# Kernel optimization log

Hardware: AMD Instinct MI355X
Metric: run time of the kernel (lower is better)

Reference implementation:

```python
import jax, jax.numpy as jnp
import numpy as np

WML, B, S, D = 64, 64, 40, 512  # word_max_len, batch, sents_max_len, dim


def setup_inputs() -> dict:
    key = jax.random.key(0)
    ks = jax.random.split(key, 8)
    source = jax.random.normal(ks[0], (B, D), dtype=jnp.float32)
    word_bank = jax.random.normal(ks[1], (WML, B, S, D), dtype=jnp.float32)
    # per-sentence word counts in [1, WML] so every sentence has >=1 valid token
    word_lengths = jax.random.randint(ks[2], (B, S), 1, WML + 1)
    sent_bank = jax.random.normal(ks[3], (S, B, D), dtype=jnp.float32)
    sent_lengths = jax.random.randint(ks[4], (B,), 1, S + 1)  # unused by forward math
    static_attn = jax.random.uniform(ks[5], (B, S), dtype=jnp.float32)
    scale = 1.0 / np.sqrt(D)
    W_word = jax.random.normal(ks[6], (D, D), dtype=jnp.float32) * scale
    W_sent = jax.random.normal(ks[7], (D, D), dtype=jnp.float32) * scale
    W_out = jax.random.normal(jax.random.fold_in(key, 99), (D, 2 * D), dtype=jnp.float32) * scale
    return {"source": source, "word_bank": word_bank, "word_lengths": word_lengths,
            "sent_bank": sent_bank, "sent_lengths": sent_lengths, "static_attn": static_attn,
            "W_word": W_word, "W_sent": W_sent, "W_out": W_out}


def reference(source, word_bank, word_lengths, sent_bank, sent_lengths, static_attn, W_word, W_sent, W_out):
    wml, batch, sents, dim = word_bank.shape
    # [wml, B, S, D] -> [B, S, wml, D] -> [B, S*wml, D]  (matches torch transpose chain)
    wb = jnp.transpose(word_bank, (1, 2, 0, 3)).reshape(batch, sents * wml, dim)
    # score(source, wb, 'word'): (source @ W_word^T) dotted with each word vector
    word_align = jnp.einsum('bd,bnd->bn', source @ W_word.T, wb)          # [B, S*wml]
    sb = jnp.transpose(sent_bank, (1, 0, 2))                               # [B, S, D]
    sent_align = jnp.einsum('bd,bsd->bs', source @ W_sent.T, sb)          # [B, S]
    # triple product: word score * sentence score * static attention
    align = (word_align.reshape(batch, sents, wml)
             * (sent_align * static_attn)[:, :, None]).reshape(batch, sents * wml)
    # sequence mask per sentence, flattened to [B, S*wml]
    mask = (jnp.arange(wml)[None, None, :] < word_lengths[:, :, None]).reshape(batch, sents * wml)
    align = jnp.where(mask, align, -jnp.inf)
    align_vectors = jax.nn.softmax(align, axis=-1) + 1e-20               # [B, S*wml]
    c = jnp.einsum('bn,bnd->bd', align_vectors, wb)                       # [B, D]
    attn_h = jnp.tanh(jnp.concatenate([c, source], axis=-1) @ W_out.T)    # [B, D]
    return attn_h, align_vectors
```

## Files before the change

kernel.cpp:

```cpp
#include <hip/hip_runtime.h>
#include <math.h>

#define BB   64
#define SS   40
#define WMLC 64
#define DD   512
#define NN   2560
#define NBLK 20
#define WPB  4
#define NWAVES (NBLK*WPB)
#define RPW (NN/NWAVES)
#define L2E 1.4426950408889634f

__device__ __forceinline__ float wave_reduce_sum(float v) {
    #pragma unroll
    for (int off = 32; off > 0; off >>= 1) v += __shfl_xor(v, off, 64);
    return v;
}

__global__ __launch_bounds__(256) void k_proj(const float* __restrict__ src,
                                              const float* __restrict__ Ww,
                                              const float* __restrict__ Ws,
                                              float* __restrict__ qw,
                                              float* __restrict__ qs) {
    __shared__ float xs[DD];
    const int b = blockIdx.y;
    const int t = threadIdx.x;
    const float* W = blockIdx.x ? Ws : Ww;
    float* q = blockIdx.x ? qs : qw;
    ((float2*)xs)[t] = ((const float2*)(src + b * DD))[t];
    __syncthreads();
    const float* r0 = W + (size_t)t * DD;
    const float* r1 = W + (size_t)(t + 256) * DD;
    float acc0 = 0.f, acc1 = 0.f;
    for (int k = 0; k < DD; k += 4) {
        float4 x  = *(const float4*)(xs + k);
        float4 w0 = *(const float4*)(r0 + k);
        float4 w1 = *(const float4*)(r1 + k);
        acc0 += x.x * w0.x + x.y * w0.y + x.z * w0.z + x.w * w0.w;
        acc1 += x.x * w1.x + x.y * w1.y + x.z * w1.z + x.w * w1.w;
    }
    q[b * DD + t] = acc0;
    q[b * DD + t + 256] = acc1;
}

__global__ __launch_bounds__(256) void k_sstat(const float* __restrict__ qs,
                                               const float* __restrict__ sb,
                                               const float* __restrict__ sa,
                                               float* __restrict__ sstat) {
    const int b = blockIdx.x;
    const int t = threadIdx.x, wave = t >> 6, lane = t & 63;
    const int d0 = lane * 4, d1 = 256 + lane * 4;
    const float4 q0 = *(const float4*)(qs + b * DD + d0);
    const float4 q1 = *(const float4*)(qs + b * DD + d1);
    for (int j = 0; j < SS / WPB; ++j) {
        const int s = wave * (SS / WPB) + j;
        const float* row = sb + ((size_t)s * BB + b) * DD;
        float4 a0 = *(const float4*)(row + d0);
        float4 a1 = *(const float4*)(row + d1);
        float p = a0.x * q0.x + a0.y * q0.y + a0.z * q0.z + a0.w * q0.w
                + a1.x * q1.x + a1.y * q1.y + a1.z * q1.z + a1.w * q1.w;
        p = wave_reduce_sum(p);
        if (lane == 0) sstat[b * SS + s] = p * sa[b * SS + s];
    }
}

__global__ __launch_bounds__(256) void k_main(const float* __restrict__ wb,
                                              const float* __restrict__ qw,
                                              const float* __restrict__ sstat,
                                              const int* __restrict__ wl,
                                              float* __restrict__ scores,
                                              float* __restrict__ part_c,
                                              float* __restrict__ part_ml) {
    const int b = blockIdx.y;
    const int chunk = blockIdx.x;
    const int t = threadIdx.x, wave = t >> 6, lane = t & 63;
    const int gw = chunk * WPB + wave;
    const int d0 = lane * 4, d1 = 256 + lane * 4;
    const float4 q0 = *(const float4*)(qw + b * DD + d0);
    const float4 q1 = *(const float4*)(qw + b * DD + d1);

    float m = -INFINITY, l = 0.f;
    float4 c0 = {0.f, 0.f, 0.f, 0.f}, c1 = {0.f, 0.f, 0.f, 0.f};

    for (int k = 0; k < RPW; ++k) {
        const int n = gw + k * NWAVES;
        const int s = n >> 6, w = n & 63;
        if (w >= wl[b * SS + s]) continue;
        const float* row = wb + (size_t)(((w * BB + b) * SS + s)) * DD;
        float4 a0 = *(const float4*)(row + d0);
        float4 a1 = *(const float4*)(row + d1);
        float p = a0.x * q0.x + a0.y * q0.y + a0.z * q0.z + a0.w * q0.w
                + a1.x * q1.x + a1.y * q1.y + a1.z * q1.z + a1.w * q1.w;
        p = wave_reduce_sum(p);
        const float a = p * sstat[b * SS + s];
        if (lane == 0) scores[b * NN + n] = a;
        if (a > m) {
            const float sc = (m == -INFINITY) ? 0.f : exp2f((m - a) * L2E);
            l *= sc;
            c0.x *= sc; c0.y *= sc; c0.z *= sc; c0.w *= sc;
            c1.x *= sc; c1.y *= sc; c1.z *= sc; c1.w *= sc;
            m = a;
        }
        const float e = exp2f((a - m) * L2E);
        l += e;
        c0.x += e * a0.x; c0.y += e * a0.y; c0.z += e * a0.z; c0.w += e * a0.w;
        c1.x += e * a1.x; c1.y += e * a1.y; c1.z += e * a1.z; c1.w += e * a1.w;
    }

    __shared__ float s_m[WPB], s_l[WPB];
    __shared__ float s_c[WPB][DD];
    *(float4*)(&s_c[wave][d0]) = c0;
    *(float4*)(&s_c[wave][d1]) = c1;
    if (lane == 0) { s_m[wave] = m; s_l[wave] = l; }
    __syncthreads();
    const float mb = fmaxf(fmaxf(s_m[0], s_m[1]), fmaxf(s_m[2], s_m[3]));
    float lb = 0.f, cA = 0.f, cB = 0.f;
    #pragma unroll
    for (int wv = 0; wv < WPB; ++wv) {
        const float mi = s_m[wv];
        const float sc = (mi == -INFINITY) ? 0.f : exp2f((mi - mb) * L2E);
        lb += s_l[wv] * sc;
        cA += s_c[wv][t] * sc;
        cB += s_c[wv][t + 256] * sc;
    }
    const int pidx = b * NBLK + chunk;
    part_c[(size_t)pidx * DD + t] = cA;
    part_c[(size_t)pidx * DD + t + 256] = cB;
    if (t == 0) { part_ml[pidx * 2] = mb; part_ml[pidx * 2 + 1] = lb; }
}

__global__ __launch_bounds__(256) void k_reduce(const float* __restrict__ part_c,
                                                const float* __restrict__ part_ml,
                                                float* __restrict__ c_final,
                                                float* __restrict__ mz) {
    const int b = blockIdx.x, t = threadIdx.x;
    float mg = -INFINITY;
    for (int i = 0; i < NBLK; ++i) mg = fmaxf(mg, part_ml[(b * NBLK + i) * 2]);
    float Z = 0.f, cA = 0.f, cB = 0.f;
    for (int i = 0; i < NBLK; ++i) {
        const float mi = part_ml[(b * NBLK + i) * 2];
        const float li = part_ml[(b * NBLK + i) * 2 + 1];
        const float sc = (mi == -INFINITY) ? 0.f : exp2f((mi - mg) * L2E);
        Z += li * sc;
        cA += part_c[(size_t)(b * NBLK + i) * DD + t] * sc;
        cB += part_c[(size_t)(b * NBLK + i) * DD + t + 256] * sc;
    }
    const float invZ = 1.0f / Z;
    c_final[b * DD + t] = cA * invZ;
    c_final[b * DD + t + 256] = cB * invZ;
    if (t == 0) { mz[b * 2] = mg; mz[b * 2 + 1] = invZ; }
}

__global__ __launch_bounds__(256) void k_align(const int* __restrict__ wl,
                                               const float* __restrict__ mz,
                                               float* __restrict__ av) {
    const int b = blockIdx.y;
    const int n = blockIdx.x * 256 + threadIdx.x;
    const int s = n >> 6, w = n & 63;
    const int len = wl[b * SS + s];
    float v = 1e-20f;
    if (w < len) {
        const float a = av[b * NN + n];
        v = exp2f((a - mz[b * 2]) * L2E) * mz[b * 2 + 1] + 1e-20f;
    }
    av[b * NN + n] = v;
}

__global__ __launch_bounds__(256) void k_attnh(const float* __restrict__ c_final,
                                               const float* __restrict__ src,
                                               const float* __restrict__ Wout,
                                               float* __restrict__ out) {
    __shared__ float xs[2 * DD];
    const int b = blockIdx.y, t = threadIdx.x;
    ((float2*)xs)[t] = ((const float2*)(c_final + b * DD))[t];
    ((float2*)(xs + DD))[t] = ((const float2*)(src + b * DD))[t];
    __syncthreads();
    const int d = blockIdx.x * 256 + t;
    const float* row = Wout + (size_t)d * (2 * DD);
    float acc = 0.f;
    for (int k = 0; k < 2 * DD; k += 4) {
        float4 x = *(const float4*)(xs + k);
        float4 w = *(const float4*)(row + k);
        acc += x.x * w.x + x.y * w.y + x.z * w.z + x.w * w.w;
    }
    out[b * DD + d] = tanhf(acc);
}

extern "C" void kernel_launch(void* const* d_in, const int* in_sizes, int n_in,
                              void* d_out, int out_size, void* d_ws, size_t ws_size,
                              hipStream_t stream) {
    const float* src = (const float*)d_in[0];
    const float* wb  = (const float*)d_in[1];
    const int*   wl  = (const int*)  d_in[2];
    const float* sb  = (const float*)d_in[3];
    const float* sa  = (const float*)d_in[5];
    const float* Ww  = (const float*)d_in[6];
    const float* Wsn = (const float*)d_in[7];
    const float* Wo  = (const float*)d_in[8];
    float* out = (float*)d_out;

    float* ws = (float*)d_ws;
    float* qw      = ws;
    float* qs      = ws + 32768;
    float* sstat   = ws + 65536;
    float* part_c  = ws + 68096;
    float* part_ml = ws + 723456;
    float* mz      = ws + 726016;
    float* c_final = ws + 726144;

    float* scores = out + BB * DD;

    hipLaunchKernelGGL(k_proj,   dim3(2, BB),       dim3(256), 0, stream, src, Ww, Wsn, qw, qs);
    hipLaunchKernelGGL(k_sstat,  dim3(BB),          dim3(256), 0, stream, qs, sb, sa, sstat);
    hipLaunchKernelGGL(k_main,   dim3(NBLK, BB),    dim3(256), 0, stream, wb, qw, sstat, wl,
                       scores, part_c, part_ml);
    hipLaunchKernelGGL(k_reduce, dim3(BB),          dim3(256), 0, stream, part_c, part_ml, c_final, mz);
    hipLaunchKernelGGL(k_align,  dim3(NN / 256, BB), dim3(256), 0, stream, wl, mz, scores);
    hipLaunchKernelGGL(k_attnh,  dim3(2, BB),       dim3(256), 0, stream, c_final, src, Wo, out);
}
```

Baseline: 518.9 us.

## Fuse sentence-score into projection, prefetch word rows, merge align and output kernels

Folds the sentence-score computation into the projection kernel using a shared-memory query, and merges the align-normalisation and output-projection kernels into one launch, cutting the launch count from six to four. The main streaming loop now caches word lengths and sentence scores in shared memory and software-prefetches the next valid word row while the current one is processed, to hide global-load latency. The cost is more register pressure in the main loop and some divergent block roles in the fused kernels.

```diff
diff --git a/kernel.cpp b/kernel.cpp
--- a/kernel.cpp
+++ b/kernel.cpp
@@ -10,6 +10,7 @@
 #define WPB  4
 #define NWAVES (NBLK*WPB)
 #define RPW (NN/NWAVES)
+#define ABLK (NN/256)
 #define L2E 1.4426950408889634f
 
 __device__ __forceinline__ float wave_reduce_sum(float v) {
@@ -21,13 +22,16 @@
 __global__ __launch_bounds__(256) void k_proj(const float* __restrict__ src,
                                               const float* __restrict__ Ww,
                                               const float* __restrict__ Ws,
+                                              const float* __restrict__ sb,
+                                              const float* __restrict__ sa,
                                               float* __restrict__ qw,
-                                              float* __restrict__ qs) {
+                                              float* __restrict__ sstat) {
     __shared__ float xs[DD];
+    __shared__ float qsl[DD];
     const int b = blockIdx.y;
     const int t = threadIdx.x;
-    const float* W = blockIdx.x ? Ws : Ww;
-    float* q = blockIdx.x ? qs : qw;
+    const bool sent = blockIdx.x != 0;
+    const float* W = sent ? Ws : Ww;
     ((float2*)xs)[t] = ((const float2*)(src + b * DD))[t];
     __syncthreads();
     const float* r0 = W + (size_t)t * DD;
@@ -40,19 +44,18 @@
         acc0 += x.x * w0.x + x.y * w0.y + x.z * w0.z + x.w * w0.w;
         acc1 += x.x * w1.x + x.y * w1.y + x.z * w1.z + x.w * w1.w;
     }
-    q[b * DD + t] = acc0;
-    q[b * DD + t + 256] = acc1;
-}
-
-__global__ __launch_bounds__(256) void k_sstat(const float* __restrict__ qs,
-                                               const float* __restrict__ sb,
-                                               const float* __restrict__ sa,
-                                               float* __restrict__ sstat) {
-    const int b = blockIdx.x;
-    const int t = threadIdx.x, wave = t >> 6, lane = t & 63;
+    if (!sent) {
+        qw[b * DD + t] = acc0;
+        qw[b * DD + t + 256] = acc1;
+        return;
+    }
+    qsl[t] = acc0;
+    qsl[t + 256] = acc1;
+    __syncthreads();
+    const int wave = t >> 6, lane = t & 63;
     const int d0 = lane * 4, d1 = 256 + lane * 4;
-    const float4 q0 = *(const float4*)(qs + b * DD + d0);
-    const float4 q1 = *(const float4*)(qs + b * DD + d1);
+    const float4 q0 = *(const float4*)(qsl + d0);
+    const float4 q1 = *(const float4*)(qsl + d1);
     for (int j = 0; j < SS / WPB; ++j) {
         const int s = wave * (SS / WPB) + j;
         const float* row = sb + ((size_t)s * BB + b) * DD;
@@ -65,6 +68,26 @@
     }
 }
 
+#define PROCESS_ROW()                                                          \
+    {                                                                          \
+        float p = p0.x * qa0.x + p0.y * qa0.y + p0.z * qa0.z + p0.w * qa0.w    \
+                + p1.x * qa1.x + p1.y * qa1.y + p1.z * qa1.z + p1.w * qa1.w;   \
+        p = wave_reduce_sum(p);                                                \
+        const float a = p * s_st[pn >> 6];                                     \
+        if (lane == 0) scores[b * NN + pn] = a;                                \
+        if (a > m) {                                                           \
+            const float sc = (m == -INFINITY) ? 0.f : exp2f((m - a) * L2E);    \
+            l *= sc;                                                           \
+            c0.x *= sc; c0.y *= sc; c0.z *= sc; c0.w *= sc;                    \
+            c1.x *= sc; c1.y *= sc; c1.z *= sc; c1.w *= sc;                    \
+            m = a;                                                             \
+        }                                                                      \
+        const float e = exp2f((a - m) * L2E);                                  \
+        l += e;                                                                \
+        c0.x += e * p0.x; c0.y += e * p0.y; c0.z += e * p0.z; c0.w += e * p0.w;\
+        c1.x += e * p1.x; c1.y += e * p1.y; c1.z += e * p1.z; c1.w += e * p1.w;\
+    }
+
 __global__ __launch_bounds__(256) void k_main(const float* __restrict__ wb,
                                               const float* __restrict__ qw,
                                               const float* __restrict__ sstat,
@@ -72,44 +95,54 @@
                                               float* __restrict__ scores,
                                               float* __restrict__ part_c,
                                               float* __restrict__ part_ml) {
+    __shared__ int   s_wl[SS];
+    __shared__ float s_st[SS];
+    __shared__ float s_m[WPB], s_l[WPB];
+    __shared__ float s_c[WPB][DD];
     const int b = blockIdx.y;
     const int chunk = blockIdx.x;
     const int t = threadIdx.x, wave = t >> 6, lane = t & 63;
+    if (t < SS) {
+        s_wl[t] = wl[b * SS + t];
+        s_st[t] = sstat[b * SS + t];
+    }
     const int gw = chunk * WPB + wave;
     const int d0 = lane * 4, d1 = 256 + lane * 4;
-    const float4 q0 = *(const float4*)(qw + b * DD + d0);
-    const float4 q1 = *(const float4*)(qw + b * DD + d1);
+    const float4 qa0 = *(const float4*)(qw + b * DD + d0);
+    const float4 qa1 = *(const float4*)(qw + b * DD + d1);
+    __syncthreads();
 
     float m = -INFINITY, l = 0.f;
     float4 c0 = {0.f, 0.f, 0.f, 0.f}, c1 = {0.f, 0.f, 0.f, 0.f};
 
-    for (int k = 0; k < RPW; ++k) {
+    int    pn = -1;
+    float4 p0 = {0.f, 0.f, 0.f, 0.f}, p1 = {0.f, 0.f, 0.f, 0.f};
+
+    int k = 0;
+    for (; k < RPW; ++k) {
         const int n = gw + k * NWAVES;
         const int s = n >> 6, w = n & 63;
-        if (w >= wl[b * SS + s]) continue;
-        const float* row = wb + (size_t)(((w * BB + b) * SS + s)) * DD;
-        float4 a0 = *(const float4*)(row + d0);
-        float4 a1 = *(const float4*)(row + d1);
-        float p = a0.x * q0.x + a0.y * q0.y + a0.z * q0.z + a0.w * q0.w
-                + a1.x * q1.x + a1.y * q1.y + a1.z * q1.z + a1.w * q1.w;
-        p = wave_reduce_sum(p);
-        const float a = p * sstat[b * SS + s];
-        if (lane == 0) scores[b * NN + n] = a;
-        if (a > m) {
-            const float sc = (m == -INFINITY) ? 0.f : exp2f((m - a) * L2E);
-            l *= sc;
-            c0.x *= sc; c0.y *= sc; c0.z *= sc; c0.w *= sc;
-            c1.x *= sc; c1.y *= sc; c1.z *= sc; c1.w *= sc;
-            m = a;
+        if (w < s_wl[s]) {
+            const float* row = wb + (size_t)((w * BB + b) * SS + s) * DD;
+            p0 = *(const float4*)(row + d0);
+            p1 = *(const float4*)(row + d1);
+            pn = n;
+            ++k;
+            break;
         }
-        const float e = exp2f((a - m) * L2E);
-        l += e;
-        c0.x += e * a0.x; c0.y += e * a0.y; c0.z += e * a0.z; c0.w += e * a0.w;
-        c1.x += e * a1.x; c1.y += e * a1.y; c1.z += e * a1.z; c1.w += e * a1.w;
-    }
-
-    __shared__ float s_m[WPB], s_l[WPB];
-    __shared__ float s_c[WPB][DD];
+    }
+    for (; k < RPW; ++k) {
+        const int n = gw + k * NWAVES;
+        const int s = n >> 6, w = n & 63;
+        if (w >= s_wl[s]) continue;
+        const float* row = wb + (size_t)((w * BB + b) * SS + s) * DD;
+        const float4 f0 = *(const float4*)(row + d0);
+        const float4 f1 = *(const float4*)(row + d1);
+        PROCESS_ROW();
+        p0 = f0; p1 = f1; pn = n;
+    }
+    if (pn >= 0) PROCESS_ROW();
+
     *(float4*)(&s_c[wave][d0]) = c0;
     *(float4*)(&s_c[wave][d1]) = c1;
     if (lane == 0) { s_m[wave] = m; s_l[wave] = l; }
@@ -152,31 +185,32 @@
     if (t == 0) { mz[b * 2] = mg; mz[b * 2 + 1] = invZ; }
 }
 
-__global__ __launch_bounds__(256) void k_align(const int* __restrict__ wl,
-                                               const float* __restrict__ mz,
-                                               float* __restrict__ av) {
+__global__ __launch_bounds__(256) void k_fin(const int* __restrict__ wl,
+                                             const float* __restrict__ mz,
+                                             float* __restrict__ av,
+                                             const float* __restrict__ c_final,
+                                             const float* __restrict__ src,
+                                             const float* __restrict__ Wout,
+                                             float* __restrict__ out) {
+    __shared__ float xs[2 * DD];
     const int b = blockIdx.y;
-    const int n = blockIdx.x * 256 + threadIdx.x;
-    const int s = n >> 6, w = n & 63;
-    const int len = wl[b * SS + s];
-    float v = 1e-20f;
-    if (w < len) {
-        const float a = av[b * NN + n];
-        v = exp2f((a - mz[b * 2]) * L2E) * mz[b * 2 + 1] + 1e-20f;
-    }
-    av[b * NN + n] = v;
-}
-
-__global__ __launch_bounds__(256) void k_attnh(const float* __restrict__ c_final,
-                                               const float* __restrict__ src,
-                                               const float* __restrict__ Wout,
-                                               float* __restrict__ out) {
-    __shared__ float xs[2 * DD];
-    const int b = blockIdx.y, t = threadIdx.x;
+    const int t = threadIdx.x;
+    if (blockIdx.x < ABLK) {
+        const int n = blockIdx.x * 256 + t;
+        const int s = n >> 6, w = n & 63;
+        const int len = wl[b * SS + s];
+        float v = 1e-20f;
+        if (w < len) {
+            const float a = av[b * NN + n];
+            v = exp2f((a - mz[b * 2]) * L2E) * mz[b * 2 + 1] + 1e-20f;
+        }
+        av[b * NN + n] = v;
+        return;
+    }
     ((float2*)xs)[t] = ((const float2*)(c_final + b * DD))[t];
     ((float2*)(xs + DD))[t] = ((const float2*)(src + b * DD))[t];
     __syncthreads();
-    const int d = blockIdx.x * 256 + t;
+    const int d = (blockIdx.x - ABLK) * 256 + t;
     const float* row = Wout + (size_t)d * (2 * DD);
     float acc = 0.f;
     for (int k = 0; k < 2 * DD; k += 4) {
@@ -202,20 +236,20 @@
 
     float* ws = (float*)d_ws;
     float* qw      = ws;
-    float* qs      = ws + 32768;
-    float* sstat   = ws + 65536;
-    float* part_c  = ws + 68096;
-    float* part_ml = ws + 723456;
-    float* mz      = ws + 726016;
-    float* c_final = ws + 726144;
+    float* sstat   = ws + 32768;
+    float* part_c  = ws + 35328;
+    float* part_ml = ws + 690688;
+    float* mz      = ws + 693248;
+    float* c_final = ws + 693376;
 
     float* scores = out + BB * DD;
 
-    hipLaunchKernelGGL(k_proj,   dim3(2, BB),       dim3(256), 0, stream, src, Ww, Wsn, qw, qs);
-    hipLaunchKernelGGL(k_sstat,  dim3(BB),          dim3(256), 0, stream, qs, sb, sa, sstat);
-    hipLaunchKernelGGL(k_main,   dim3(NBLK, BB),    dim3(256), 0, stream, wb, qw, sstat, wl,
-                       scores, part_c, part_ml);
-    hipLaunchKernelGGL(k_reduce, dim3(BB),          dim3(256), 0, stream, part_c, part_ml, c_final, mz);
-    hipLaunchKernelGGL(k_align,  dim3(NN / 256, BB), dim3(256), 0, stream, wl, mz, scores);
-    hipLaunchKernelGGL(k_attnh,  dim3(2, BB),       dim3(256), 0, stream, c_final, src, Wo, out);
-}
+    hipLaunchKernelGGL(k_proj,   dim3(2, BB),        dim3(256), 0, stream,
+                       src, Ww, Wsn, sb, sa, qw, sstat);
+    hipLaunchKernelGGL(k_main,   dim3(NBLK, BB),     dim3(256), 0, stream,
+                       wb, qw, sstat, wl, scores, part_c, part_ml);
+    hipLaunchKernelGGL(k_reduce, dim3(BB),           dim3(256), 0, stream,
+                       part_c, part_ml, c_final, mz);
+    hipLaunchKernelGGL(k_fin,    dim3(ABLK + 2, BB), dim3(256), 0, stream,
+                       wl, mz, scores, c_final, src, Wo, out);
+}
```

After: 513.5 us. Within noise of the previous version (-1.1%).
